# Optimization experiments

Hardware: AMD Instinct MI355X
Metric: run time of the kernel (lower is better)

The kernel has to match this reference:

```python
import jax, jax.numpy as jnp
import numpy as np

NUM_LEVELS = 3
B, T, D, H = 512, 2048, 64, 32


def _uni(k, shape, fan_in):
    s = 1.0 / np.sqrt(fan_in)
    return jax.random.uniform(k, shape, jnp.float32, -s, s)


def setup_inputs() -> dict:
    key = jax.random.key(0)
    ks = jax.random.split(key, 10)
    lw = jnp.linspace(1.0, float(NUM_LEVELS), NUM_LEVELS)
    lw = lw / lw.sum()
    return {
        "latent_ys": jax.random.normal(ks[0], (B, T, D), jnp.float32),
        "Wx": _uni(ks[1], (D, H), D), "bx": _uni(ks[2], (H,), D),
        "Wu": _uni(ks[3], (D, H), D), "bu": _uni(ks[4], (H,), D),
        "Ws": _uni(ks[5], (2 * H, 1), 2 * H), "bs": _uni(ks[6], (1,), 2 * H),
        "level_weights": lw,
        "Wf": _uni(ks[7], (2 * D, D), 2 * D), "bf": _uni(ks[8], (D,), 2 * D),
        "gamma": jnp.ones((D,), jnp.float32),
        "beta": jnp.zeros((D,), jnp.float32),
    }


def reference(latent_ys, Wx, bx, Wu, bu, Ws, bs, level_weights, Wf, bf, gamma, beta):
    Bn, Tn, Dn = latent_ys.shape
    x_repr = latent_ys[:, 0, :]          # (B,D)
    u_repr = latent_ys.mean(axis=1)       # (B,D)

    # Eq. 8-9 attention: score_net is linear on concat, so S[i,j] = ex_i.w1 + eu_j.w2 + b
    ex = x_repr @ Wx + bx                 # (B,H)
    eu = u_repr @ Wu + bu                 # (B,H)
    Hn = ex.shape[-1]
    S = (ex @ Ws[:Hn, 0])[:, None] + (eu @ Ws[Hn:, 0])[None, :] + bs[0]
    eye = jnp.eye(Bn, dtype=bool)
    S = jnp.where(eye, -jnp.inf, S)
    weights = jax.nn.softmax(S, axis=-1)  # (B,B), diag = 0

    # pyramidal sort (Algorithm 1), vectorized over the batch dim
    other = ~eye
    active = other
    dt = latent_ys.dtype
    levels = []
    for _ in range(NUM_LEVELS - 1):
        cnt = active.sum(-1, keepdims=True).astype(dt)                         # (B,1)
        asum = jnp.sum(jnp.where(active, weights, 0.0), -1, keepdims=True)      # (B,1)
        mean_val = asum / jnp.maximum(cnt, 1.0)
        lower = active & (weights <= mean_val)                                  # (B,B)
        lcnt = lower.sum(-1).astype(dt)[:, None]                                # (B,1)
        lsum = lower.astype(dt) @ u_repr                                        # (B,D)
        levels.append(jnp.where(lcnt > 0, lsum / jnp.maximum(lcnt, 1.0), 0.0))
        active = active & ~lower
    acnt = active.sum(-1).astype(dt)[:, None]
    asum_r = active.astype(dt) @ u_repr
    top_idx = jnp.argmax(jnp.where(other, weights, -1.0), axis=-1)              # (B,)
    fallback = u_repr[top_idx]
    levels.append(jnp.where(acnt > 0, asum_r / jnp.maximum(acnt, 1.0), fallback))
    level_reprs = jnp.stack(levels, axis=1)                                     # (B,L,D)

    cross = jnp.einsum('bld,l->bd', level_reprs, level_weights)                 # (B,D)
    # fusion Linear on concat([latent_ys, cross]) split into two GEMMs
    fused = latent_ys @ Wf[:Dn] + (cross @ Wf[Dn:] + bf)[:, None, :]           # (B,T,D)
    y = fused + latent_ys
    mu = y.mean(-1, keepdims=True)
    var = y.var(-1, keepdims=True)
    return gamma * (y - mu) * jax.lax.rsqrt(var + 1e-5) + beta
```

## Files before the change

### kernel.cpp

```cpp
#include <hip/hip_runtime.h>

typedef unsigned short ushort_t;
typedef __attribute__((ext_vector_type(8))) short short8;
typedef __attribute__((ext_vector_type(4))) float f32x4;

#define BB 512
#define TT 2048
#define DD 64

__device__ __forceinline__ ushort_t f2b(float f) {
    union { float f; unsigned int i; } v; v.f = f;
    unsigned int u = v.i;
    unsigned int r = (u + 0x7fffu + ((u >> 16) & 1u)) >> 16;
    return (ushort_t)r;
}

__global__ __launch_bounds__(1024) void k_umean(const float* __restrict__ lat,
                                                const float* __restrict__ Wu,
                                                const float* __restrict__ Ws,
                                                float* __restrict__ u,
                                                float* __restrict__ bj) {
    int b = blockIdx.x;
    int tid = threadIdx.x;
    int cg = tid & 15;
    int rs = tid >> 4;
    const float* base = lat + (size_t)b * TT * DD;
    float acc[4] = {0.f, 0.f, 0.f, 0.f};
#pragma unroll 4
    for (int k = 0; k < 32; k++) {
        int r = rs + 64 * k;
        float4 vv = *reinterpret_cast<const float4*>(base + (size_t)r * DD + cg * 4);
        acc[0] += vv.x; acc[1] += vv.y; acc[2] += vv.z; acc[3] += vv.w;
    }
    __shared__ float sm[64][64];
#pragma unroll
    for (int j = 0; j < 4; j++) sm[rs][cg * 4 + j] = acc[j];
    __syncthreads();
    {
        int col = tid & 63, g = tid >> 6;
        float p = 0.0f;
#pragma unroll
        for (int k = 0; k < 4; k++) p += sm[g + 16 * k][col];
        sm[g][col] = p;
    }
    __syncthreads();
    if (tid < 64) {
        float tot = 0.0f;
#pragma unroll
        for (int g = 0; g < 16; g++) tot += sm[g][tid];
        float um = tot * (1.0f / (float)TT);
        u[(size_t)b * DD + tid] = um;
        float vv = 0.0f;
#pragma unroll
        for (int h = 0; h < 32; h++) vv += Wu[tid * 32 + h] * Ws[32 + h];
        float p = um * vv;
#pragma unroll
        for (int m = 1; m < 64; m <<= 1) p += __shfl_xor(p, m, 64);
        if (tid == 0) bj[b] = p;
    }
}

__global__ __launch_bounds__(64) void k_stats(const float* __restrict__ bj,
                                              float* __restrict__ E,
                                              float* __restrict__ miscf,
                                              int* __restrict__ misci) {
    int lane = threadIdx.x;
    float vals[8];
#pragma unroll
    for (int k = 0; k < 8; k++) vals[k] = bj[lane + 64 * k];
    float mx = vals[0]; int mi = lane;
#pragma unroll
    for (int k = 1; k < 8; k++) {
        int j = lane + 64 * k;
        if (vals[k] > mx) { mx = vals[k]; mi = j; }
    }
#pragma unroll
    for (int m = 1; m < 64; m <<= 1) {
        float om = __shfl_xor(mx, m, 64);
        int oi = __shfl_xor(mi, m, 64);
        if (om > mx || (om == mx && oi < mi)) { mx = om; mi = oi; }
    }
    int j1 = mi; float maxb = mx;
    float mx2 = -3.4e38f; int mi2 = 0x7fffffff;
#pragma unroll
    for (int k = 0; k < 8; k++) {
        int j = lane + 64 * k;
        float t = (j == j1) ? -3.4e38f : vals[k];
        if (t > mx2 || (t == mx2 && j < mi2)) { mx2 = t; mi2 = j; }
    }
#pragma unroll
    for (int m = 1; m < 64; m <<= 1) {
        float om = __shfl_xor(mx2, m, 64);
        int oi = __shfl_xor(mi2, m, 64);
        if (om > mx2 || (om == mx2 && oi < mi2)) { mx2 = om; mi2 = oi; }
    }
    float zs = 0.0f;
#pragma unroll
    for (int k = 0; k < 8; k++) {
        float e = expf(vals[k] - maxb);
        E[lane + 64 * k] = e;
        zs += e;
    }
#pragma unroll
    for (int m = 1; m < 64; m <<= 1) zs += __shfl_xor(zs, m, 64);
    if (lane == 0) { miscf[0] = zs; misci[1] = j1; misci[2] = mi2; }
}

__global__ __launch_bounds__(256) void k_levels(const float* __restrict__ u,
                                                const float* __restrict__ E,
                                                const float* __restrict__ miscf,
                                                const int* __restrict__ misci,
                                                const float* __restrict__ lw,
                                                const float* __restrict__ Wf,
                                                const float* __restrict__ bfv,
                                                float* __restrict__ cbias) {
    int i = blockIdx.x;
    int tid = threadIdx.x;
    int lane = tid & 63, wv = tid >> 6;
    __shared__ signed char lvl[512];
    __shared__ float red[16];
    __shared__ __align__(16) float lr[16][3][64];
    __shared__ float crossS[64];

    float Z = miscf[0];
    float Ei = E[i];
    float denom = Z - Ei;
    int jA = tid, jB = tid + 256;
    float wA = (jA == i) ? 0.0f : (E[jA] / denom);
    float wB = (jB == i) ? 0.0f : (E[jB] / denom);

    float s = wA + wB;
#pragma unroll
    for (int m = 1; m < 64; m <<= 1) s += __shfl_xor(s, m, 64);
    if (lane == 0) red[wv] = s;
    __syncthreads();
    float mean0 = (red[0] + red[1] + red[2] + red[3]) * (1.0f / 511.0f);

    float pa = 0.0f, ca = 0.0f, c1 = 0.0f;
    if (jA != i) { if (wA <= mean0) c1 += 1.0f; else { pa += wA; ca += 1.0f; } }
    if (jB != i) { if (wB <= mean0) c1 += 1.0f; else { pa += wB; ca += 1.0f; } }
#pragma unroll
    for (int m = 1; m < 64; m <<= 1) {
        pa += __shfl_xor(pa, m, 64);
        ca += __shfl_xor(ca, m, 64);
        c1 += __shfl_xor(c1, m, 64);
    }
    if (lane == 0) { red[4 + wv] = pa; red[8 + wv] = ca; red[12 + wv] = c1; }
    __syncthreads();
    float asum1 = red[4] + red[5] + red[6] + red[7];
    float cact  = red[8] + red[9] + red[10] + red[11];
    float cnt1  = red[12] + red[13] + red[14] + red[15];
    float mean1 = asum1 / fmaxf(cact, 1.0f);

    float c2 = 0.0f;
    signed char lA, lB;
    if (jA == i) lA = -1;
    else if (wA <= mean0) lA = 0;
    else if (wA <= mean1) { lA = 1; c2 += 1.0f; }
    else lA = 2;
    if (jB == i) lB = -1;
    else if (wB <= mean0) lB = 0;
    else if (wB <= mean1) { lB = 1; c2 += 1.0f; }
    else lB = 2;
    lvl[jA] = lA; lvl[jB] = lB;
#pragma unroll
    for (int m = 1; m < 64; m <<= 1) c2 += __shfl_xor(c2, m, 64);
    if (lane == 0) red[wv] = c2;
    __syncthreads();
    float cnt2 = red[0] + red[1] + red[2] + red[3];
    float cnt3 = cact - cnt2;

    int jg = tid >> 4;
    int d4 = (tid & 15) << 2;
    float4 a0 = make_float4(0.f, 0.f, 0.f, 0.f);
    float4 a1 = make_float4(0.f, 0.f, 0.f, 0.f);
    float4 a2 = make_float4(0.f, 0.f, 0.f, 0.f);
#pragma unroll 8
    for (int j = jg; j < 512; j += 16) {
        int l = lvl[j];
        float4 uv = *reinterpret_cast<const float4*>(u + (size_t)j * DD + d4);
        if (l == 0) { a0.x += uv.x; a0.y += uv.y; a0.z += uv.z; a0.w += uv.w; }
        else if (l == 1) { a1.x += uv.x; a1.y += uv.y; a1.z += uv.z; a1.w += uv.w; }
        else if (l == 2) { a2.x += uv.x; a2.y += uv.y; a2.z += uv.z; a2.w += uv.w; }
    }
    *reinterpret_cast<float4*>(&lr[jg][0][d4]) = a0;
    *reinterpret_cast<float4*>(&lr[jg][1][d4]) = a1;
    *reinterpret_cast<float4*>(&lr[jg][2][d4]) = a2;
    __syncthreads();

    if (tid < 64) {
        float s0 = 0.0f, s1 = 0.0f, s2 = 0.0f;
#pragma unroll
        for (int g2 = 0; g2 < 16; g2++) {
            s0 += lr[g2][0][tid];
            s1 += lr[g2][1][tid];
            s2 += lr[g2][2][tid];
        }
        int j1 = misci[1], j2 = misci[2];
        int fb = (j1 == i) ? j2 : j1;
        float L1 = (cnt1 > 0.0f) ? s0 / cnt1 : 0.0f;
        float L2 = (cnt2 > 0.0f) ? s1 / cnt2 : 0.0f;
        float L3 = (cnt3 > 0.0f) ? s2 / cnt3 : u[(size_t)fb * DD + tid];
        crossS[tid] = lw[0] * L1 + lw[1] * L2 + lw[2] * L3;
    }
    __syncthreads();
    if (tid < 64) {
        int n = tid;
        float sacc = 0.0f;
        for (int dd = 0; dd < 64; dd++) sacc += crossS[dd] * Wf[(64 + dd) * 64 + n];
        cbias[(size_t)i * DD + n] = sacc + bfv[n];
    }
}

__global__ __launch_bounds__(256) void k_fused(const float* __restrict__ lat,
                                               const float* __restrict__ Wf,
                                               const float* __restrict__ cbias,
                                               const float* __restrict__ gamma,
                                               const float* __restrict__ beta,
                                               float* __restrict__ out) {
    int tid = threadIdx.x;
    int lane = tid & 63, wv = tid >> 6;
    int lo = lane & 15, quad = lane >> 4;
    long wid = (long)blockIdx.x * 4 + wv;

    short8 bfr[4][2];
#pragma unroll
    for (int c = 0; c < 4; c++) {
        int n = 16 * c + lo;
#pragma unroll
        for (int s = 0; s < 2; s++) {
            short8 t;
#pragma unroll
            for (int j = 0; j < 8; j++) {
                int k = 32 * s + 8 * quad + j;
                float vv = Wf[k * 64 + n] + (k == n ? 1.0f : 0.0f);
                t[j] = (short)f2b(vv);
            }
            bfr[c][s] = t;
        }
    }
    float ga[4], be[4], cb[4];
    int b = (int)(wid >> 5);
#pragma unroll
    for (int c = 0; c < 4; c++) {
        int n = 16 * c + lo;
        ga[c] = gamma[n];
        be[c] = beta[n];
        cb[c] = cbias[(size_t)b * DD + n];
    }

    for (int t4 = 0; t4 < 4; t4++) {
        long row0 = (wid * 4 + t4) * 16;
        const float* ap = lat + (size_t)(row0 + lo) * DD + quad * 8;
        float4 f0 = *reinterpret_cast<const float4*>(ap);
        float4 f1 = *reinterpret_cast<const float4*>(ap + 4);
        float4 f2 = *reinterpret_cast<const float4*>(ap + 32);
        float4 f3 = *reinterpret_cast<const float4*>(ap + 36);
        short8 a0, a1;
        a0[0] = (short)f2b(f0.x); a0[1] = (short)f2b(f0.y);
        a0[2] = (short)f2b(f0.z); a0[3] = (short)f2b(f0.w);
        a0[4] = (short)f2b(f1.x); a0[5] = (short)f2b(f1.y);
        a0[6] = (short)f2b(f1.z); a0[7] = (short)f2b(f1.w);
        a1[0] = (short)f2b(f2.x); a1[1] = (short)f2b(f2.y);
        a1[2] = (short)f2b(f2.z); a1[3] = (short)f2b(f2.w);
        a1[4] = (short)f2b(f3.x); a1[5] = (short)f2b(f3.y);
        a1[6] = (short)f2b(f3.z); a1[7] = (short)f2b(f3.w);

        f32x4 acc[4];
#pragma unroll
        for (int c = 0; c < 4; c++) { acc[c] = (f32x4){0.f, 0.f, 0.f, 0.f}; }
#pragma unroll
        for (int c = 0; c < 4; c++) {
            acc[c] = __builtin_amdgcn_mfma_f32_16x16x32_bf16(a0, bfr[c][0], acc[c], 0, 0, 0);
            acc[c] = __builtin_amdgcn_mfma_f32_16x16x32_bf16(a1, bfr[c][1], acc[c], 0, 0, 0);
        }
        float y[4][4];
#pragma unroll
        for (int c = 0; c < 4; c++)
#pragma unroll
            for (int r = 0; r < 4; r++) y[c][r] = acc[c][r] + cb[c];
#pragma unroll
        for (int r = 0; r < 4; r++) {
            float s = y[0][r] + y[1][r] + y[2][r] + y[3][r];
            float q = y[0][r] * y[0][r] + y[1][r] * y[1][r] + y[2][r] * y[2][r] + y[3][r] * y[3][r];
#pragma unroll
            for (int m = 1; m < 16; m <<= 1) {
                s += __shfl_xor(s, m, 64);
                q += __shfl_xor(q, m, 64);
            }
            float mean = s * (1.0f / 64.0f);
            float var = q * (1.0f / 64.0f) - mean * mean;
            float rstd = rsqrtf(var + 1e-5f);
            long row = row0 + quad * 4 + r;
#pragma unroll
            for (int c = 0; c < 4; c++) {
                float o = ga[c] * (y[c][r] - mean) * rstd + be[c];
                out[(size_t)row * DD + 16 * c + lo] = o;
            }
        }
    }
}

extern "C" void kernel_launch(void* const* d_in, const int* in_sizes, int n_in,
                              void* d_out, int out_size, void* d_ws, size_t ws_size,
                              hipStream_t stream) {
    const float* lat   = (const float*)d_in[0];
    const float* Wu    = (const float*)d_in[3];
    const float* Ws    = (const float*)d_in[5];
    const float* lw    = (const float*)d_in[7];
    const float* Wf    = (const float*)d_in[8];
    const float* bfv   = (const float*)d_in[9];
    const float* gamma = (const float*)d_in[10];
    const float* beta  = (const float*)d_in[11];
    float* out = (float*)d_out;

    char* ws = (char*)d_ws;
    float* u     = (float*)(ws);
    float* bjv   = (float*)(ws + 131072);
    float* E     = (float*)(ws + 133120);
    float* miscf = (float*)(ws + 135168);
    int*   misci = (int*)(ws + 135168);
    float* cbias = (float*)(ws + 135424);

    k_umean<<<BB, 1024, 0, stream>>>(lat, Wu, Ws, u, bjv);
    k_stats<<<1, 64, 0, stream>>>(bjv, E, miscf, misci);
    k_levels<<<BB, 256, 0, stream>>>(u, E, miscf, misci, lw, Wf, bfv, cbias);
    k_fused<<<4096, 256, 0, stream>>>(lat, Wf, cbias, gamma, beta, out);
}
```

Measured before the change: 539.6 us.

## Precast activations to bf16 in mean pass and fold softmax stats into levels

The mean-reduction kernel now also writes a bf16 copy of the input activations to workspace. The fused GEMM+LayerNorm kernel then loads these half-width values directly instead of loading fp32 and converting per element. The single-block stats kernel is removed: each levels block recomputes the softmax max, second max and partition sum from the score vector, which saves one launch and one dependency step. Total DRAM traffic stays about the same, because the first pass gains a large extra write stream, so any benefit depends on cache reuse of the bf16 copy and on lighter conversion work in the GEMM kernel.

```diff
diff --git a/kernel.cpp b/kernel.cpp
--- a/kernel.cpp
+++ b/kernel.cpp
@@ -19,18 +19,23 @@
                                                 const float* __restrict__ Wu,
                                                 const float* __restrict__ Ws,
                                                 float* __restrict__ u,
-                                                float* __restrict__ bj) {
+                                                float* __restrict__ bj,
+                                                ushort_t* __restrict__ latb) {
     int b = blockIdx.x;
     int tid = threadIdx.x;
     int cg = tid & 15;
     int rs = tid >> 4;
     const float* base = lat + (size_t)b * TT * DD;
+    ushort_t* bbase = latb + (size_t)b * TT * DD;
     float acc[4] = {0.f, 0.f, 0.f, 0.f};
 #pragma unroll 4
     for (int k = 0; k < 32; k++) {
         int r = rs + 64 * k;
         float4 vv = *reinterpret_cast<const float4*>(base + (size_t)r * DD + cg * 4);
         acc[0] += vv.x; acc[1] += vv.y; acc[2] += vv.z; acc[3] += vv.w;
+        ushort4 sv;
+        sv.x = f2b(vv.x); sv.y = f2b(vv.y); sv.z = f2b(vv.z); sv.w = f2b(vv.w);
+        *reinterpret_cast<ushort4*>(bbase + (size_t)r * DD + cg * 4) = sv;
     }
     __shared__ float sm[64][64];
 #pragma unroll
@@ -60,56 +65,8 @@
     }
 }
 
-__global__ __launch_bounds__(64) void k_stats(const float* __restrict__ bj,
-                                              float* __restrict__ E,
-                                              float* __restrict__ miscf,
-                                              int* __restrict__ misci) {
-    int lane = threadIdx.x;
-    float vals[8];
-#pragma unroll
-    for (int k = 0; k < 8; k++) vals[k] = bj[lane + 64 * k];
-    float mx = vals[0]; int mi = lane;
-#pragma unroll
-    for (int k = 1; k < 8; k++) {
-        int j = lane + 64 * k;
-        if (vals[k] > mx) { mx = vals[k]; mi = j; }
-    }
-#pragma unroll
-    for (int m = 1; m < 64; m <<= 1) {
-        float om = __shfl_xor(mx, m, 64);
-        int oi = __shfl_xor(mi, m, 64);
-        if (om > mx || (om == mx && oi < mi)) { mx = om; mi = oi; }
-    }
-    int j1 = mi; float maxb = mx;
-    float mx2 = -3.4e38f; int mi2 = 0x7fffffff;
-#pragma unroll
-    for (int k = 0; k < 8; k++) {
-        int j = lane + 64 * k;
-        float t = (j == j1) ? -3.4e38f : vals[k];
-        if (t > mx2 || (t == mx2 && j < mi2)) { mx2 = t; mi2 = j; }
-    }
-#pragma unroll
-    for (int m = 1; m < 64; m <<= 1) {
-        float om = __shfl_xor(mx2, m, 64);
-        int oi = __shfl_xor(mi2, m, 64);
-        if (om > mx2 || (om == mx2 && oi < mi2)) { mx2 = om; mi2 = oi; }
-    }
-    float zs = 0.0f;
-#pragma unroll
-    for (int k = 0; k < 8; k++) {
-        float e = expf(vals[k] - maxb);
-        E[lane + 64 * k] = e;
-        zs += e;
-    }
-#pragma unroll
-    for (int m = 1; m < 64; m <<= 1) zs += __shfl_xor(zs, m, 64);
-    if (lane == 0) { miscf[0] = zs; misci[1] = j1; misci[2] = mi2; }
-}
-
 __global__ __launch_bounds__(256) void k_levels(const float* __restrict__ u,
-                                                const float* __restrict__ E,
-                                                const float* __restrict__ miscf,
-                                                const int* __restrict__ misci,
+                                                const float* __restrict__ bj,
                                                 const float* __restrict__ lw,
                                                 const float* __restrict__ Wf,
                                                 const float* __restrict__ bfv,
@@ -118,23 +75,67 @@
     int tid = threadIdx.x;
     int lane = tid & 63, wv = tid >> 6;
     __shared__ signed char lvl[512];
-    __shared__ float red[16];
+    __shared__ float redf[16];
+    __shared__ int redi[8];
     __shared__ __align__(16) float lr[16][3][64];
     __shared__ float crossS[64];
 
-    float Z = miscf[0];
-    float Ei = E[i];
+    int jA = tid, jB = tid + 256;
+    float vA = bj[jA], vB = bj[jB];
+
+    float mx; int mi;
+    if (vB > vA) { mx = vB; mi = jB; } else { mx = vA; mi = jA; }
+#pragma unroll
+    for (int m = 1; m < 64; m <<= 1) {
+        float om = __shfl_xor(mx, m, 64);
+        int oi = __shfl_xor(mi, m, 64);
+        if (om > mx || (om == mx && oi < mi)) { mx = om; mi = oi; }
+    }
+    if (lane == 0) { redf[wv] = mx; redi[wv] = mi; }
+    __syncthreads();
+    float maxb = redf[0]; int j1 = redi[0];
+#pragma unroll
+    for (int w2 = 1; w2 < 4; w2++) {
+        float om = redf[w2]; int oi = redi[w2];
+        if (om > maxb || (om == maxb && oi < j1)) { maxb = om; j1 = oi; }
+    }
+
+    float eA = expf(vA - maxb), eB = expf(vB - maxb);
+    float zs = eA + eB;
+    float mx2; int mi2;
+    {
+        float tA = (jA == j1) ? -3.4e38f : vA;
+        float tB = (jB == j1) ? -3.4e38f : vB;
+        if (tB > tA) { mx2 = tB; mi2 = jB; } else { mx2 = tA; mi2 = jA; }
+    }
+#pragma unroll
+    for (int m = 1; m < 64; m <<= 1) {
+        float om = __shfl_xor(mx2, m, 64);
+        int oi = __shfl_xor(mi2, m, 64);
+        if (om > mx2 || (om == mx2 && oi < mi2)) { mx2 = om; mi2 = oi; }
+        zs += __shfl_xor(zs, m, 64);
+    }
+    if (lane == 0) { redf[4 + wv] = mx2; redi[4 + wv] = mi2; redf[8 + wv] = zs; }
+    __syncthreads();
+    float Z = redf[8] + redf[9] + redf[10] + redf[11];
+    int j2 = redi[4]; float m2v = redf[4];
+#pragma unroll
+    for (int w2 = 1; w2 < 4; w2++) {
+        float om = redf[4 + w2]; int oi = redi[4 + w2];
+        if (om > m2v || (om == m2v && oi < j2)) { m2v = om; j2 = oi; }
+    }
+
+    float Ei = expf(bj[i] - maxb);
     float denom = Z - Ei;
-    int jA = tid, jB = tid + 256;
-    float wA = (jA == i) ? 0.0f : (E[jA] / denom);
-    float wB = (jB == i) ? 0.0f : (E[jB] / denom);
+    float wA = (jA == i) ? 0.0f : (eA / denom);
+    float wB = (jB == i) ? 0.0f : (eB / denom);
 
     float s = wA + wB;
 #pragma unroll
     for (int m = 1; m < 64; m <<= 1) s += __shfl_xor(s, m, 64);
-    if (lane == 0) red[wv] = s;
-    __syncthreads();
-    float mean0 = (red[0] + red[1] + red[2] + red[3]) * (1.0f / 511.0f);
+    if (lane == 0) redf[wv] = s;
+    __syncthreads();
+    float mean0 = (redf[0] + redf[1] + redf[2] + redf[3]) * (1.0f / 511.0f);
 
     float pa = 0.0f, ca = 0.0f, c1 = 0.0f;
     if (jA != i) { if (wA <= mean0) c1 += 1.0f; else { pa += wA; ca += 1.0f; } }
@@ -145,11 +146,11 @@
         ca += __shfl_xor(ca, m, 64);
         c1 += __shfl_xor(c1, m, 64);
     }
-    if (lane == 0) { red[4 + wv] = pa; red[8 + wv] = ca; red[12 + wv] = c1; }
-    __syncthreads();
-    float asum1 = red[4] + red[5] + red[6] + red[7];
-    float cact  = red[8] + red[9] + red[10] + red[11];
-    float cnt1  = red[12] + red[13] + red[14] + red[15];
+    if (lane == 0) { redf[4 + wv] = pa; redf[8 + wv] = ca; redf[12 + wv] = c1; }
+    __syncthreads();
+    float asum1 = redf[4] + redf[5] + redf[6] + redf[7];
+    float cact  = redf[8] + redf[9] + redf[10] + redf[11];
+    float cnt1  = redf[12] + redf[13] + redf[14] + redf[15];
     float mean1 = asum1 / fmaxf(cact, 1.0f);
 
     float c2 = 0.0f;
@@ -165,9 +166,9 @@
     lvl[jA] = lA; lvl[jB] = lB;
 #pragma unroll
     for (int m = 1; m < 64; m <<= 1) c2 += __shfl_xor(c2, m, 64);
-    if (lane == 0) red[wv] = c2;
-    __syncthreads();
-    float cnt2 = red[0] + red[1] + red[2] + red[3];
+    if (lane == 0) redf[wv] = c2;
+    __syncthreads();
+    float cnt2 = redf[0] + redf[1] + redf[2] + redf[3];
     float cnt3 = cact - cnt2;
 
     int jg = tid >> 4;
@@ -196,7 +197,6 @@
             s1 += lr[g2][1][tid];
             s2 += lr[g2][2][tid];
         }
-        int j1 = misci[1], j2 = misci[2];
         int fb = (j1 == i) ? j2 : j1;
         float L1 = (cnt1 > 0.0f) ? s0 / cnt1 : 0.0f;
         float L2 = (cnt2 > 0.0f) ? s1 / cnt2 : 0.0f;
@@ -212,7 +212,7 @@
     }
 }
 
-__global__ __launch_bounds__(256) void k_fused(const float* __restrict__ lat,
+__global__ __launch_bounds__(256) void k_fused(const ushort_t* __restrict__ latb,
                                                const float* __restrict__ Wf,
                                                const float* __restrict__ cbias,
                                                const float* __restrict__ gamma,
@@ -251,20 +251,9 @@
 
     for (int t4 = 0; t4 < 4; t4++) {
         long row0 = (wid * 4 + t4) * 16;
-        const float* ap = lat + (size_t)(row0 + lo) * DD + quad * 8;
-        float4 f0 = *reinterpret_cast<const float4*>(ap);
-        float4 f1 = *reinterpret_cast<const float4*>(ap + 4);
-        float4 f2 = *reinterpret_cast<const float4*>(ap + 32);
-        float4 f3 = *reinterpret_cast<const float4*>(ap + 36);
-        short8 a0, a1;
-        a0[0] = (short)f2b(f0.x); a0[1] = (short)f2b(f0.y);
-        a0[2] = (short)f2b(f0.z); a0[3] = (short)f2b(f0.w);
-        a0[4] = (short)f2b(f1.x); a0[5] = (short)f2b(f1.y);
-        a0[6] = (short)f2b(f1.z); a0[7] = (short)f2b(f1.w);
-        a1[0] = (short)f2b(f2.x); a1[1] = (short)f2b(f2.y);
-        a1[2] = (short)f2b(f2.z); a1[3] = (short)f2b(f2.w);
-        a1[4] = (short)f2b(f3.x); a1[5] = (short)f2b(f3.y);
-        a1[6] = (short)f2b(f3.z); a1[7] = (short)f2b(f3.w);
+        const ushort_t* ap = latb + (size_t)(row0 + lo) * DD + quad * 8;
+        short8 a0 = *reinterpret_cast<const short8*>(ap);
+        short8 a1 = *reinterpret_cast<const short8*>(ap + 32);
 
         f32x4 acc[4];
 #pragma unroll
@@ -315,15 +304,12 @@
     float* out = (float*)d_out;
 
     char* ws = (char*)d_ws;
-    float* u     = (float*)(ws);
-    float* bjv   = (float*)(ws + 131072);
-    float* E     = (float*)(ws + 133120);
-    float* miscf = (float*)(ws + 135168);
-    int*   misci = (int*)(ws + 135168);
-    float* cbias = (float*)(ws + 135424);
-
-    k_umean<<<BB, 1024, 0, stream>>>(lat, Wu, Ws, u, bjv);
-    k_stats<<<1, 64, 0, stream>>>(bjv, E, miscf, misci);
-    k_levels<<<BB, 256, 0, stream>>>(u, E, miscf, misci, lw, Wf, bfv, cbias);
-    k_fused<<<4096, 256, 0, stream>>>(lat, Wf, cbias, gamma, beta, out);
-}
+    float*    u     = (float*)(ws);
+    float*    bjv   = (float*)(ws + 131072);
+    float*    cbias = (float*)(ws + 133120);
+    ushort_t* latb  = (ushort_t*)(ws + 264192);
+
+    k_umean<<<BB, 1024, 0, stream>>>(lat, Wu, Ws, u, bjv, latb);
+    k_levels<<<BB, 256, 0, stream>>>(u, bjv, lw, Wf, bfv, cbias);
+    k_fused<<<4096, 256, 0, stream>>>(latb, Wf, cbias, gamma, beta, out);
+}
```

New measurement: 554.2 us. +2.7%, slower.
